# Kernel tuning notes

Hardware: AMD Instinct MI355X
Metric: run time of the kernel (lower is better)

Reference implementation:

```python
import jax, jax.numpy as jnp
import numpy as np

B, MAX_H, MAX_W, D, S, HID = 64, 64, 32, 512, 8, 64


def setup_inputs() -> dict:
    key = jax.random.key(0)
    ks = jax.random.split(key, 7)
    return {
        "canonical": jax.random.normal(ks[0], (S, S, D), jnp.float32) * 0.02,
        "w1": jax.random.normal(ks[1], (2, HID), jnp.float32) * 0.5,
        "b1": jax.random.normal(ks[2], (HID,), jnp.float32) * 0.1,
        "w2": jax.random.normal(ks[3], (HID, D), jnp.float32) * 0.05,
        "b2": jax.random.normal(ks[4], (D,), jnp.float32) * 0.05,
        "batch_size": B,
        "target_h_list": jax.random.randint(ks[5], (B,), 1, MAX_H + 1, jnp.int32),
        "target_w_list": jax.random.randint(ks[6], (B,), 1, MAX_W + 1, jnp.int32),
        "max_h": MAX_H,
        "max_w": MAX_W,
    }


def _axis_coords(sizes, max_len):
    # sizes: [B] clamped lengths; returns normalized coords u in [0,1] at each
    # padded position (torch.linspace(0,1,L) semantics; 0 when L==1). [B, max_len]
    idx = jnp.arange(max_len, dtype=jnp.float32)[None, :]
    L = sizes[:, None].astype(jnp.float32)
    return jnp.where(L > 1, idx / jnp.maximum(L - 1.0, 1.0), 0.0)


def _forward(canonical, w1, b1, w2, b2, target_h_list, target_w_list, max_h, max_w):
    S_ = canonical.shape[0]
    Hs = jnp.clip(target_h_list, 1, max_h)  # [B]
    Ws = jnp.clip(target_w_list, 1, max_w)  # [B]

    u = _axis_coords(Hs, max_h)  # [B, mh]
    v = _axis_coords(Ws, max_w)  # [B, mw]

    # Bilinear resize of canonical grid with align_corners=True:
    # source coord = normalized coord * (S-1)
    sy = jnp.clip(u * (S_ - 1), 0.0, S_ - 1.0)  # [B, mh]
    sx = jnp.clip(v * (S_ - 1), 0.0, S_ - 1.0)  # [B, mw]
    y0 = jnp.floor(sy).astype(jnp.int32)
    x0 = jnp.floor(sx).astype(jnp.int32)
    y1 = jnp.minimum(y0 + 1, S_ - 1)
    x1 = jnp.minimum(x0 + 1, S_ - 1)
    wy = (sy - y0.astype(jnp.float32))[:, :, None, None]  # [B, mh, 1, 1]
    wx = (sx - x0.astype(jnp.float32))[:, None, :, None]  # [B, 1, mw, 1]

    yi0 = y0[:, :, None]  # [B, mh, 1]
    yi1 = y1[:, :, None]
    xi0 = x0[:, None, :]  # [B, 1, mw]
    xi1 = x1[:, None, :]
    q00 = canonical[yi0, xi0]  # [B, mh, mw, D]
    q01 = canonical[yi0, xi1]
    q10 = canonical[yi1, xi0]
    q11 = canonical[yi1, xi1]
    bil = ((1.0 - wy) * ((1.0 - wx) * q00 + wx * q01)
           + wy * ((1.0 - wx) * q10 + wx * q11))  # [B, mh, mw, D]

    # Coordinate refinement MLP on (u, v)
    coords = jnp.stack(
        [jnp.broadcast_to(u[:, :, None], (u.shape[0], max_h, max_w)),
         jnp.broadcast_to(v[:, None, :], (u.shape[0], max_h, max_w))],
        axis=-1)  # [B, mh, mw, 2]
    h = jax.nn.gelu(coords @ w1 + b1, approximate=False)
    delta = h @ w2 + b2  # [B, mh, mw, D]

    mask = ((jnp.arange(max_h)[None, :, None] < Hs[:, None, None])
            & (jnp.arange(max_w)[None, None, :] < Ws[:, None, None]))  # [B, mh, mw]
    queries = jnp.where(mask[..., None], bil + delta, 0.0)
    return queries, mask


def reference(canonical, w1, b1, w2, b2, batch_size, target_h_list,
              target_w_list, max_h, max_w):
    return _forward(canonical, w1, b1, w2, b2, target_h_list, target_w_list,
                    max_h, max_w)
```

## Files before the change

kernel.cpp:

```cpp
#include <hip/hip_runtime.h>
#include <math.h>

#define NB    64
#define MAXH  64
#define MAXW  32
#define DCH   512
#define SS    8
#define HID   64

#define QTOTAL ((size_t)NB * MAXH * MAXW * DCH)

typedef float f4 __attribute__((ext_vector_type(4)));

__device__ __forceinline__ float gelu_exact(float x) {
    return 0.5f * x * (1.0f + erff(x * 0.70710678118654752440f));
}

__global__ __launch_bounds__(256) void hgqg_kernel(
    const float* __restrict__ canonical,
    const float* __restrict__ w1,
    const float* __restrict__ b1,
    const float* __restrict__ w2,
    const float* __restrict__ b2,
    const int*   __restrict__ hlist,
    const int*   __restrict__ wlist,
    float* __restrict__ out)
{
    const int raw  = blockIdx.x;
    const int id   = (raw ^ (raw >> 7)) & 8191;
    const int i    = id & 63;
    const int half = (id >> 6) & 1;
    const int b    = id >> 7;
    const int blk  = (b << 6) | i;
    const int t    = threadIdx.x;

    int H = hlist[b]; H = min(max(H, 1), MAXH);
    int W = wlist[b]; W = min(max(W, 1), MAXW);

    const int jbase = half << 4;

    f4* q4 = (f4*)(out + (size_t)blk * (MAXW * DCH)) + jbase * 128;

    if (half == 0 && t < MAXW) {
        out[QTOTAL + (size_t)blk * MAXW + t] = (i < H && t < W) ? 1.0f : 0.0f;
    }

    const f4 z = {0.f, 0.f, 0.f, 0.f};

    if (i >= H || jbase >= W) {
        #pragma unroll
        for (int r = 0; r < 8; ++r) q4[t + r * 256] = z;
        return;
    }

    const float u    = (H > 1) ? (float)i / (float)(H - 1) : 0.0f;
    const float sy   = fminf(u * 7.0f, 7.0f);
    const int   y0   = (int)sy;
    const int   y1   = min(y0 + 1, SS - 1);
    const float wy   = sy - (float)y0;
    const float winv = (W > 1) ? 1.0f / (float)(W - 1) : 0.0f;

    __shared__ __align__(16) float hsh[16][HID];
    {
        const int jl = t >> 4;
        const int k0 = (t & 15) * 4;
        const float v = (float)(jbase + jl) * winv;
        #pragma unroll
        for (int kk = 0; kk < 4; ++kk) {
            const int k = k0 + kk;
            hsh[jl][k] = gelu_exact(u * w1[k] + v * w1[HID + k] + b1[k]);
        }
    }
    __syncthreads();

    const int cid = t & 127;
    const int jg  = t >> 7;
    const f4  bb2 = ((const f4*)b2)[cid];
    const f4* can4 = (const f4*)canonical;
    const f4* wp   = (const f4*)w2 + cid;

    f4 acc[8];
    #pragma unroll
    for (int s = 0; s < 8; ++s) acc[s] = z;

    if (jbase + jg < W) {
        #pragma unroll
        for (int s = 0; s < 8; ++s) {
            const int j = jbase + jg + 2 * s;
            if (j < W) {
                const float v  = (float)j * winv;
                const float sx = fminf(v * 7.0f, 7.0f);
                const int   x0 = (int)sx;
                const int   x1 = min(x0 + 1, SS - 1);
                const float wx = sx - (float)x0;
                const f4 q00 = can4[(y0 * SS + x0) * 128 + cid];
                const f4 q01 = can4[(y0 * SS + x1) * 128 + cid];
                const f4 q10 = can4[(y1 * SS + x0) * 128 + cid];
                const f4 q11 = can4[(y1 * SS + x1) * 128 + cid];
                const f4 t0 = q00 + wx * (q01 - q00);
                const f4 t1 = q10 + wx * (q11 - q10);
                acc[s] = t0 + wy * (t1 - t0) + bb2;
            }
        }
        #pragma unroll 1
        for (int kb = 0; kb < HID; kb += 4) {
            const f4 wa = wp[(kb + 0) * 128];
            const f4 wb = wp[(kb + 1) * 128];
            const f4 wc = wp[(kb + 2) * 128];
            const f4 wd = wp[(kb + 3) * 128];
            #pragma unroll
            for (int s = 0; s < 8; ++s) {
                const int j = jbase + jg + 2 * s;
                if (j < W) {
                    const int jl = jg + 2 * s;
                    const f4 h4 = *(const f4*)&hsh[jl][kb];
                    acc[s] += h4.x * wa + h4.y * wb + h4.z * wc + h4.w * wd;
                }
            }
        }
    }

    #pragma unroll
    for (int s = 0; s < 8; ++s) {
        const int j = jg + 2 * s;
        q4[j * 128 + cid] = acc[s];
    }
}

extern "C" void kernel_launch(void* const* d_in, const int* in_sizes, int n_in,
                              void* d_out, int out_size, void* d_ws, size_t ws_size,
                              hipStream_t stream) {
    const float* canonical = (const float*)d_in[0];
    const float* w1        = (const float*)d_in[1];
    const float* b1        = (const float*)d_in[2];
    const float* w2        = (const float*)d_in[3];
    const float* b2        = (const float*)d_in[4];
    const int*   hlist     = (const int*)d_in[6];
    const int*   wlist     = (const int*)d_in[7];
    float* out = (float*)d_out;

    hgqg_kernel<<<2 * NB * MAXH, 256, 0, stream>>>(
        canonical, w1, b1, w2, b2, hlist, wlist, out);
}
```

Measured before the change: 306.9 us.

## Compute MLP second layer with bf16 MFMA and stage row-interpolated canonical in LDS

A small pre-kernel converts w2 to bf16 and packs it into the MFMA B-operand layout in the workspace. The main kernel does the 16x64 by 64x512 hidden projection with two 16x16x32 bf16 MFMAs per channel tile, in place of scalar FMA loops. It also precomputes the y-interpolated canonical rows once per block in shared memory, so the per-output bilinear step becomes one x-lerp read from LDS. The outputs are now written as scalar stores, and casting the GELU activations and w2 to bf16 lowers precision.

```diff
diff --git a/kernel.cpp b/kernel.cpp
--- a/kernel.cpp
+++ b/kernel.cpp
@@ -10,17 +10,43 @@
 
 #define QTOTAL ((size_t)NB * MAXH * MAXW * DCH)
 
-typedef float f4 __attribute__((ext_vector_type(4)));
+typedef float f4  __attribute__((ext_vector_type(4)));
+typedef short s8v __attribute__((ext_vector_type(8)));
 
 __device__ __forceinline__ float gelu_exact(float x) {
     return 0.5f * x * (1.0f + erff(x * 0.70710678118654752440f));
+}
+
+__device__ __forceinline__ unsigned short bf16_rne(float x) {
+    unsigned int u = __float_as_uint(x);
+    unsigned int r = u + 0x7fffu + ((u >> 16) & 1u);
+    return (unsigned short)(r >> 16);
+}
+
+__global__ __launch_bounds__(256) void w2prep_kernel(
+    const float* __restrict__ w2, s8v* __restrict__ w2b)
+{
+    const int tid  = blockIdx.x * 256 + threadIdx.x;
+    const int lane = tid & 63;
+    const int ct   = (tid >> 6) & 31;
+    const int kh   = tid >> 11;
+    const int q    = lane >> 4;
+    const int m    = lane & 15;
+    const int c    = ct * 16 + m;
+    union { s8v v; unsigned short us[8]; } pk;
+    #pragma unroll
+    for (int j = 0; j < 8; ++j) {
+        const int k = kh * 32 + q * 8 + j;
+        pk.us[j] = bf16_rne(w2[k * DCH + c]);
+    }
+    w2b[tid] = pk.v;
 }
 
 __global__ __launch_bounds__(256) void hgqg_kernel(
     const float* __restrict__ canonical,
     const float* __restrict__ w1,
     const float* __restrict__ b1,
-    const float* __restrict__ w2,
+    const s8v*   __restrict__ w2b,
     const float* __restrict__ b2,
     const int*   __restrict__ hlist,
     const int*   __restrict__ wlist,
@@ -60,7 +86,21 @@
     const float wy   = sy - (float)y0;
     const float winv = (W > 1) ? 1.0f / (float)(W - 1) : 0.0f;
 
-    __shared__ __align__(16) float hsh[16][HID];
+    __shared__ __align__(16) float ri[SS * 516];
+    {
+        const f4* can4 = (const f4*)canonical;
+        #pragma unroll
+        for (int rr = 0; rr < 4; ++rr) {
+            const int idx = t + rr * 256;
+            const int x   = idx >> 7;
+            const int c4  = idx & 127;
+            const f4 a = can4[(y0 * SS + x) * 128 + c4];
+            const f4 d = can4[(y1 * SS + x) * 128 + c4];
+            *(f4*)&ri[x * 516 + c4 * 4] = a + wy * (d - a);
+        }
+    }
+
+    __shared__ __align__(16) float hsh[16][68];
     {
         const int jl = t >> 4;
         const int k0 = (t & 15) * 4;
@@ -73,57 +113,60 @@
     }
     __syncthreads();
 
-    const int cid = t & 127;
-    const int jg  = t >> 7;
-    const f4  bb2 = ((const f4*)b2)[cid];
-    const f4* can4 = (const f4*)canonical;
-    const f4* wp   = (const f4*)w2 + cid;
+    const int l = t & 63;
+    const int w = t >> 6;
+    const int q = l >> 4;
+    const int m = l & 15;
 
-    f4 acc[8];
-    #pragma unroll
-    for (int s = 0; s < 8; ++s) acc[s] = z;
-
-    if (jbase + jg < W) {
+    union { s8v v; unsigned short us[8]; } A0, A1;
+    {
+        const float* hrow = &hsh[m][q * 8];
         #pragma unroll
-        for (int s = 0; s < 8; ++s) {
-            const int j = jbase + jg + 2 * s;
-            if (j < W) {
-                const float v  = (float)j * winv;
-                const float sx = fminf(v * 7.0f, 7.0f);
-                const int   x0 = (int)sx;
-                const int   x1 = min(x0 + 1, SS - 1);
-                const float wx = sx - (float)x0;
-                const f4 q00 = can4[(y0 * SS + x0) * 128 + cid];
-                const f4 q01 = can4[(y0 * SS + x1) * 128 + cid];
-                const f4 q10 = can4[(y1 * SS + x0) * 128 + cid];
-                const f4 q11 = can4[(y1 * SS + x1) * 128 + cid];
-                const f4 t0 = q00 + wx * (q01 - q00);
-                const f4 t1 = q10 + wx * (q11 - q10);
-                acc[s] = t0 + wy * (t1 - t0) + bb2;
-            }
-        }
-        #pragma unroll 1
-        for (int kb = 0; kb < HID; kb += 4) {
-            const f4 wa = wp[(kb + 0) * 128];
-            const f4 wb = wp[(kb + 1) * 128];
-            const f4 wc = wp[(kb + 2) * 128];
-            const f4 wd = wp[(kb + 3) * 128];
-            #pragma unroll
-            for (int s = 0; s < 8; ++s) {
-                const int j = jbase + jg + 2 * s;
-                if (j < W) {
-                    const int jl = jg + 2 * s;
-                    const f4 h4 = *(const f4*)&hsh[jl][kb];
-                    acc[s] += h4.x * wa + h4.y * wb + h4.z * wc + h4.w * wd;
-                }
-            }
+        for (int j = 0; j < 8; ++j) {
+            A0.us[j] = bf16_rne(hrow[j]);
+            A1.us[j] = bf16_rne(hrow[32 + j]);
         }
     }
 
+    int   x0a[4], x1a[4];
+    float wxa[4];
     #pragma unroll
-    for (int s = 0; s < 8; ++s) {
-        const int j = jg + 2 * s;
-        q4[j * 128 + cid] = acc[s];
+    for (int r = 0; r < 4; ++r) {
+        const int   j  = jbase + q * 4 + r;
+        const float v  = (float)j * winv;
+        const float sx = fminf(v * 7.0f, 7.0f);
+        const int   x0 = (int)sx;
+        x0a[r] = x0;
+        x1a[r] = min(x0 + 1, SS - 1);
+        wxa[r] = sx - (float)x0;
+    }
+
+    const size_t obase = (size_t)blk * (MAXW * DCH) + (size_t)jbase * DCH;
+
+    #pragma unroll
+    for (int tt = 0; tt < 8; ++tt) {
+        const int ct = w * 8 + tt;
+        const int c  = ct * 16 + m;
+
+        f4 acc;
+        const float bb2 = b2[c];
+        #pragma unroll
+        for (int r = 0; r < 4; ++r) {
+            const float f0 = ri[x0a[r] * 516 + c];
+            const float f1 = ri[x1a[r] * 516 + c];
+            acc[r] = f0 + wxa[r] * (f1 - f0) + bb2;
+        }
+
+        const s8v b0 = w2b[ct * 64 + l];
+        const s8v b1f = w2b[2048 + ct * 64 + l];
+        acc = __builtin_amdgcn_mfma_f32_16x16x32_bf16(A0.v, b0, acc, 0, 0, 0);
+        acc = __builtin_amdgcn_mfma_f32_16x16x32_bf16(A1.v, b1f, acc, 0, 0, 0);
+
+        #pragma unroll
+        for (int r = 0; r < 4; ++r) {
+            const int j = jbase + q * 4 + r;
+            out[obase + (size_t)(q * 4 + r) * DCH + c] = (j < W) ? acc[r] : 0.0f;
+        }
     }
 }
 
@@ -138,7 +181,9 @@
     const int*   hlist     = (const int*)d_in[6];
     const int*   wlist     = (const int*)d_in[7];
     float* out = (float*)d_out;
+    s8v*   w2b = (s8v*)d_ws;
 
+    w2prep_kernel<<<16, 256, 0, stream>>>(w2, w2b);
     hgqg_kernel<<<2 * NB * MAXH, 256, 0, stream>>>(
-        canonical, w1, b1, w2, b2, hlist, wlist, out);
+        canonical, w1, b1, w2b, b2, hlist, wlist, out);
 }
```

After: 280.9 us. -8.5%, faster.
